# Optimization experiments

Measured on AMD Instinct MI355X. Metric: run time of the kernel, lower is better.

Reference implementation:

```python
import jax, jax.numpy as jnp
import numpy as np

D_MODEL = 1024
N_HEADS = 16
D_HEAD = D_MODEL // N_HEADS
B, T = 4, 2048


def setup_inputs() -> dict:
    key = jax.random.key(0)
    ks = jax.random.split(key, 7)
    s = 0.02
    q = jax.random.normal(ks[0], (B, T, D_MODEL), dtype=jnp.float32)
    k = jax.random.normal(ks[1], (B, T, D_MODEL), dtype=jnp.float32)
    v = jax.random.normal(ks[2], (B, T, D_MODEL), dtype=jnp.float32)
    # causal mask, True = masked (strict upper triangle)
    mask = jnp.triu(jnp.ones((T, T), dtype=bool), k=1)[None, None, :, :]
    Wq = jax.random.normal(ks[3], (D_MODEL, D_MODEL), dtype=jnp.float32) * s
    Wk = jax.random.normal(ks[4], (D_MODEL, D_MODEL), dtype=jnp.float32) * s
    Wv = jax.random.normal(ks[5], (D_MODEL, D_MODEL), dtype=jnp.float32) * s
    Wo = jax.random.normal(ks[6], (D_MODEL, D_MODEL), dtype=jnp.float32) * s
    return {"q": q, "k": k, "v": v, "mask": mask,
            "Wq": Wq, "Wk": Wk, "Wv": Wv, "Wo": Wo}


def reference(q, k, v, mask, Wq, Wk, Wv, Wo):
    H, Dh = N_HEADS, D_HEAD
    scale = Dh ** -0.5

    def split(t):  # [B,T,D] -> [B,H,T,Dh]
        Bt, Tt, _ = t.shape
        return t.reshape(Bt, Tt, H, Dh).transpose(0, 2, 1, 3)

    # torch Linear (no bias): y = x @ W.T
    Q = split(q @ Wq.T)
    K = split(k @ Wk.T)
    V = split(v @ Wv.T)

    scores = jnp.einsum('bhqd,bhkd->bhqk', Q, K) * scale
    scores = jnp.where(mask, -jnp.inf, scores)
    attn = jax.nn.softmax(scores, axis=-1)
    attn = jnp.nan_to_num(attn)  # fully-masked rows -> 0
    out = jnp.einsum('bhqk,bhkd->bhqd', attn, V)
    out = out.transpose(0, 2, 1, 3).reshape(q.shape[0], q.shape[1], H * Dh)
    return out @ Wo.T
```

## Files before the change

kernel.cpp:

```cpp
#include <hip/hip_runtime.h>
#include <stdint.h>

#define D_MODEL 1024
#define N_HEADS 16
#define D_HEAD 64
#define BATCH 4
#define SEQ 2048
#define MTOT (BATCH * SEQ)

typedef unsigned short u16;
typedef __attribute__((ext_vector_type(8))) short bf16x8;
typedef __attribute__((ext_vector_type(4))) float f32x4;

#define MFMA(a, b, c) __builtin_amdgcn_mfma_f32_16x16x32_bf16((a), (b), (c), 0, 0, 0)
#define LOG2E 1.4426950408889634f
#define SC (0.125f * LOG2E)

static __device__ __forceinline__ u16 f2bf(float f) {
  unsigned u = __builtin_bit_cast(unsigned, f);
  u += 0x7fffu + ((u >> 16) & 1u);
  return (u16)(u >> 16);
}
static __device__ __forceinline__ u16 f2bf_t(float f) {
  return (u16)(__builtin_bit_cast(unsigned, f) >> 16);
}

static __device__ __forceinline__ void gload_lds16(const void* g, void* l) {
  __builtin_amdgcn_global_load_lds(
      (const __attribute__((address_space(1))) void*)g,
      (__attribute__((address_space(3))) void*)l, 16, 0, 0);
}

__global__ __launch_bounds__(256) void cvt3(const float* __restrict__ a,
                                            const float* __restrict__ b,
                                            const float* __restrict__ c,
                                            u16* __restrict__ oa, u16* __restrict__ ob,
                                            u16* __restrict__ oc) {
  const int z = blockIdx.y;
  const float* in = (z == 0) ? a : (z == 1) ? b : c;
  u16* out = (z == 0) ? oa : (z == 1) ? ob : oc;
  int i = blockIdx.x * 256 + threadIdx.x;
  float4 v = ((const float4*)in)[i];
  ushort4 o;
  o.x = f2bf(v.x); o.y = f2bf(v.y); o.z = f2bf(v.z); o.w = f2bf(v.w);
  ((ushort4*)out)[i] = o;
}

__global__ __launch_bounds__(256) void cvt4(const float* __restrict__ a,
                                            const float* __restrict__ b,
                                            const float* __restrict__ c,
                                            const float* __restrict__ d,
                                            u16* __restrict__ oa, u16* __restrict__ ob,
                                            u16* __restrict__ oc, u16* __restrict__ od) {
  const int z = blockIdx.y;
  const float* in = (z == 0) ? a : (z == 1) ? b : (z == 2) ? c : d;
  u16* out = (z == 0) ? oa : (z == 1) ? ob : (z == 2) ? oc : od;
  const float s = (z == 0) ? SC : 1.0f;
  int i = blockIdx.x * 256 + threadIdx.x;
  float4 v = ((const float4*)in)[i];
  ushort4 o;
  o.x = f2bf(v.x * s); o.y = f2bf(v.y * s); o.z = f2bf(v.z * s); o.w = f2bf(v.w * s);
  ((ushort4*)out)[i] = o;
}

#define BM 256
#define BN 128
#define BK 64
#define NKT (D_MODEL / BK)
#define ASZ (BM * BK)
#define BSZ (BN * BK)

static __device__ __forceinline__ void gemm_core(const u16* __restrict__ A,
                                                 const u16* __restrict__ B,
                                                 u16* As, u16* Bs,
                                                 int m0, int n0, f32x4 acc[4][4]) {
  const int t = threadIdx.x;
  const int lane = t & 63, wave = t >> 6;
  const int wm = wave >> 1, wn = wave & 1;
  const int lrow = lane & 15, quad = lane >> 4;
  const int srow = t >> 3;
  const int swcol = (((t & 7) ^ (srow & 7)) << 3);
  const int sdst = srow * 64 + (t & 7) * 8;
  const int rsw = lrow & 7;

#pragma unroll
  for (int i = 0; i < 4; i++)
#pragma unroll
    for (int j = 0; j < 4; j++) acc[i][j] = (f32x4){0.f, 0.f, 0.f, 0.f};

#define STAGE_(kt_, bi_)                                                        \
  do {                                                                          \
    const int k0_ = (kt_)*BK;                                                   \
    u16* as_ = As + (bi_)*ASZ;                                                  \
    u16* bs_ = Bs + (bi_)*BSZ;                                                  \
    _Pragma("unroll") for (int r_ = 0; r_ < 4; ++r_)                            \
        gload_lds16(A + (size_t)(m0 + r_ * 64 + srow) * 1024 + k0_ + swcol,     \
                    as_ + r_ * 64 * 64 + sdst);                                 \
    _Pragma("unroll") for (int r_ = 0; r_ < 2; ++r_)                            \
        gload_lds16(B + (size_t)(n0 + r_ * 64 + srow) * 1024 + k0_ + swcol,     \
                    bs_ + r_ * 64 * 64 + sdst);                                 \
  } while (0)

  STAGE_(0, 0);
  STAGE_(1, 1);

  for (int kt = 0; kt < NKT; ++kt) {
    if (kt < NKT - 1) asm volatile("s_waitcnt vmcnt(6)" ::: "memory");
    else              asm volatile("s_waitcnt vmcnt(0)" ::: "memory");
    __builtin_amdgcn_s_barrier();
    asm volatile("" ::: "memory");

    if (kt + 2 < NKT) STAGE_(kt + 2, (kt + 2) % 3);

    const u16* as = As + (kt % 3) * ASZ;
    const u16* bs = Bs + (kt % 3) * BSZ;

    bf16x8 a[2][4], b[2][4];
#pragma unroll
    for (int ks = 0; ks < 2; ++ks) {
      const int cx = ((ks * 4 + quad) ^ rsw) << 3;
#pragma unroll
      for (int i = 0; i < 4; i++)
        a[ks][i] = *(const bf16x8*)(as + (wm * 64 + i * 16 + lrow) * 64 + cx);
#pragma unroll
      for (int j = 0; j < 4; j++)
        b[ks][j] = *(const bf16x8*)(bs + (wn * 64 + j * 16 + lrow) * 64 + cx);
    }
#pragma unroll
    for (int ks = 0; ks < 2; ++ks) {
      __builtin_amdgcn_s_setprio(1);
#pragma unroll
      for (int i = 0; i < 4; i++)
#pragma unroll
        for (int j = 0; j < 4; j++) acc[i][j] = MFMA(a[ks][i], b[ks][j], acc[i][j]);
      __builtin_amdgcn_s_setprio(0);
    }
    __builtin_amdgcn_sched_barrier(0);
  }
#undef STAGE_
}

__global__ __launch_bounds__(512, 2) void gemm_qkv(const u16* __restrict__ xq,
                                                   const u16* __restrict__ xk,
                                                   const u16* __restrict__ xv,
                                                   const u16* __restrict__ Wqb,
                                                   const u16* __restrict__ Wkb,
                                                   const u16* __restrict__ Wvb,
                                                   u16* __restrict__ Qb, u16* __restrict__ Kb,
                                                   u16* __restrict__ Vtg, int zbase) {
  __shared__ u16 As[3 * ASZ];
  __shared__ u16 Bs[3 * BSZ];
  const int z = blockIdx.z + zbase;
  const u16* A = (z == 0) ? xq : (z == 1) ? xk : xv;
  const u16* B = (z == 0) ? Wqb : (z == 1) ? Wkb : Wvb;
  const int m0 = blockIdx.x * BM, n0 = blockIdx.y * BN;

  f32x4 acc[4][4];
  gemm_core(A, B, As, Bs, m0, n0, acc);

  const int lane = threadIdx.x & 63, wave = threadIdx.x >> 6;
  const int wm = wave >> 1, wn = wave & 1;
  const int lrow = lane & 15, quad = lane >> 4;

  if (z == 2) {
    const int b = m0 >> 11;
    const int t0 = (m0 & 2047);
#pragma unroll
    for (int i = 0; i < 4; i++) {
      const int trow = t0 + wm * 64 + i * 16 + quad * 4;
#pragma unroll
      for (int j = 0; j < 4; j++) {
        const int n = n0 + wn * 64 + j * 16 + lrow;
        ushort4 pk;
        pk.x = f2bf(acc[i][j][0]); pk.y = f2bf(acc[i][j][1]);
        pk.z = f2bf(acc[i][j][2]); pk.w = f2bf(acc[i][j][3]);
        *(ushort4*)(Vtg + (size_t)b * D_MODEL * SEQ + (size_t)n * SEQ + trow) = pk;
      }
    }
  } else {
    u16* C = z ? Kb : Qb;
#pragma unroll
    for (int i = 0; i < 4; i++) {
      const int mr = m0 + wm * 64 + i * 16 + quad * 4;
#pragma unroll
      for (int j = 0; j < 4; j++) {
        const int n = n0 + wn * 64 + j * 16 + lrow;
#pragma unroll
        for (int r = 0; r < 4; r++) C[(size_t)(mr + r) * 1024 + n] = f2bf(acc[i][j][r]);
      }
    }
  }
}

__global__ __launch_bounds__(512, 2) void gemm_o(const u16* __restrict__ A,
                                                 const u16* __restrict__ B,
                                                 float* __restrict__ C) {
  __shared__ u16 As[3 * ASZ];
  __shared__ u16 Bs[3 * BSZ];
  const int m0 = blockIdx.x * BM, n0 = blockIdx.y * BN;

  f32x4 acc[4][4];
  gemm_core(A, B, As, Bs, m0, n0, acc);

  const int lane = threadIdx.x & 63, wave = threadIdx.x >> 6;
  const int wm = wave >> 1, wn = wave & 1;
  const int lrow = lane & 15, quad = lane >> 4;
#pragma unroll
  for (int i = 0; i < 4; i++) {
    const int mr = m0 + wm * 64 + i * 16 + quad * 4;
#pragma unroll
    for (int j = 0; j < 4; j++) {
      const int n = n0 + wn * 64 + j * 16 + lrow;
#pragma unroll
      for (int r = 0; r < 4; r++) C[(size_t)(mr + r) * 1024 + n] = acc[i][j][r];
    }
  }
}

__global__ __launch_bounds__(256) void attn_causal(const u16* __restrict__ Qb,
                                                   const u16* __restrict__ Kb,
                                                   const u16* __restrict__ Vtg,
                                                   u16* __restrict__ Ob) {
  __shared__ u16 QPs[128 * 64];
  __shared__ u16 Ks[3 * 64 * 64];
  __shared__ u16 Vs[3 * 64 * 64];

  const int t = threadIdx.x;
  const int lane = t & 63, wave = t >> 6;
  const int lrow = lane & 15, quad = lane >> 4;
  const int wb = wave * 32;
  const int bh = blockIdx.x;
  const int b = bh >> 4, h = bh & 15;
  const int col0 = h * 64;
  const size_t rowbase = (size_t)b * SEQ;
  const size_t vbase = (size_t)b * (size_t)D_MODEL * SEQ;
  const int srow = t >> 3;
  const int swcol = (((t & 7) ^ (srow & 7)) << 3);
  const int pchunk = (t & 7) * 8;
  const int rsw = lrow & 7;

#define KVSTAGE_(kt_, bi_)                                                      \
  do {                                                                          \
    const int j0_ = (kt_)*64;                                                   \
    u16* ks_ = Ks + (bi_)*4096;                                                 \
    u16* vs_ = Vs + (bi_)*4096;                                                 \
    _Pragma("unroll") for (int r_ = 0; r_ < 2; ++r_) {                          \
      int rr_ = r_ * 32 + srow;                                                 \
      gload_lds16(Kb + (rowbase + j0_ + rr_) * D_MODEL + col0 + swcol,          \
                  ks_ + rr_ * 64 + pchunk);                                     \
      gload_lds16(Vtg + vbase + (size_t)(col0 + rr_) * SEQ + j0_ + swcol,       \
                  vs_ + rr_ * 64 + pchunk);                                     \
    }                                                                           \
  } while (0)

  bf16x8 bOnes;
  {
    const short ov = (lrow == 0) ? (short)0x3F80 : (short)0;
#pragma unroll
    for (int e = 0; e < 8; ++e) bOnes[e] = ov;
  }

  for (int part = 0; part < 2; ++part) {
    const int qt = part ? (15 - (int)blockIdx.y) : (int)blockIdx.y;
    const int qrow0 = qt * 128;
    const int nkt = 2 * qt + 2;

#pragma unroll
    for (int r = 0; r < 4; ++r) {
      int rr = r * 32 + srow;
      gload_lds16(Qb + (rowbase + qrow0 + rr) * D_MODEL + col0 + swcol,
                  QPs + rr * 64 + pchunk);
    }
    KVSTAGE_(0, 0);
    KVSTAGE_(1, 1);

    bf16x8 bQ[2][2];
    f32x4 oacc[2][4];
    f32x4 lacc[2];
#pragma unroll
    for (int mf = 0; mf < 2; mf++) {
#pragma unroll
      for (int df = 0; df < 4; df++) oacc[mf][df] = (f32x4){0.f, 0.f, 0.f, 0.f};
      lacc[mf] = (f32x4){0.f, 0.f, 0.f, 0.f};
    }

    for (int kt = 0; kt < nkt; ++kt) {
      if (kt < nkt - 1) asm volatile("s_waitcnt vmcnt(4)" ::: "memory");
      else              asm volatile("s_waitcnt vmcnt(0)" ::: "memory");
      __builtin_amdgcn_s_barrier();
      asm volatile("" ::: "memory");

      if (kt + 2 < nkt) KVSTAGE_(kt + 2, (kt + 2) % 3);

      const u16* ksb = Ks + (kt % 3) * 4096;
      const u16* vsb = Vs + (kt % 3) * 4096;

      if (kt == 0) {
#pragma unroll
        for (int mf = 0; mf < 2; ++mf)
#pragma unroll
          for (int ks = 0; ks < 2; ++ks)
            bQ[mf][ks] = *(const bf16x8*)(QPs + (wb + mf * 16 + lrow) * 64 +
                                          (((ks * 4 + quad) ^ rsw) << 3));
      }

      const int j0 = kt * 64;
      const bool diag = (kt >= 2 * qt);
#pragma unroll
      for (int mf = 0; mf < 2; ++mf) {
        f32x4 st[4];
#pragma unroll
        for (int jf = 0; jf < 4; jf++) st[jf] = (f32x4){0.f, 0.f, 0.f, 0.f};
#pragma unroll
        for (int ks = 0; ks < 2; ++ks) {
          const int cx = ((ks * 4 + quad) ^ rsw) << 3;
#pragma unroll
          for (int jf = 0; jf < 4; jf++) {
            bf16x8 aK = *(const bf16x8*)(ksb + (jf * 16 + lrow) * 64 + cx);
            st[jf] = MFMA(aK, bQ[mf][ks], st[jf]);
          }
        }
        const int m = wb + mf * 16 + lrow;
        const int gm = qrow0 + m;
#pragma unroll
        for (int jf = 0; jf < 4; jf++) {
          ushort4 pk;
#pragma unroll
          for (int r = 0; r < 4; r++) {
            float p = __builtin_amdgcn_exp2f(st[jf][r]);
            const int gj = j0 + jf * 16 + quad * 4 + r;
            if (diag && gj > gm) p = 0.f;
            ((u16*)&pk)[r] = f2bf_t(p);
          }
          const int j = jf * 16 + quad * 4;
          *(ushort4*)(QPs + m * 64 + ((((j >> 3) ^ (m & 7)) << 3) | (j & 7))) = pk;
        }
      }

#pragma unroll
      for (int ks = 0; ks < 2; ++ks) {
        const int cx = ((ks * 4 + quad) ^ rsw) << 3;
        bf16x8 aP[2];
#pragma unroll
        for (int mf = 0; mf < 2; ++mf)
          aP[mf] = *(const bf16x8*)(QPs + (wb + mf * 16 + lrow) * 64 + cx);
        lacc[0] = MFMA(aP[0], bOnes, lacc[0]);
        lacc[1] = MFMA(aP[1], bOnes, lacc[1]);
#pragma unroll
        for (int df = 0; df < 4; df++) {
          bf16x8 bV = *(const bf16x8*)(vsb + (df * 16 + lrow) * 64 + cx);
          oacc[0][df] = MFMA(aP[0], bV, oacc[0][df]);
          oacc[1][df] = MFMA(aP[1], bV, oacc[1][df]);
        }
      }
      __builtin_amdgcn_sched_barrier(0);
    }
    __syncthreads();

    float linv[2][4];
#pragma unroll
    for (int mf = 0; mf < 2; mf++)
#pragma unroll
      for (int r = 0; r < 4; r++)
        linv[mf][r] = 1.0f / __shfl(lacc[mf][r], lane & 48);

#pragma unroll
    for (int mf = 0; mf < 2; mf++)
#pragma unroll
      for (int r = 0; r < 4; r++) {
        u16* orow = Ob + (rowbase + qrow0 + wb + mf * 16 + quad * 4 + r) * D_MODEL + col0;
#pragma unroll
        for (int df = 0; df < 4; df++)
          orow[df * 16 + lrow] = f2bf(oacc[mf][df][r] * linv[mf][r]);
      }
  }
#undef KVSTAGE_
}

extern "C" void kernel_launch(void* const* d_in, const int* in_sizes, int n_in,
                              void* d_out, int out_size, void* d_ws, size_t ws_size,
                              hipStream_t stream) {
  const float* q  = (const float*)d_in[0];
  const float* k  = (const float*)d_in[1];
  const float* v  = (const float*)d_in[2];
  const float* Wq = (const float*)d_in[4];
  const float* Wk = (const float*)d_in[5];
  const float* Wv = (const float*)d_in[6];
  const float* Wo = (const float*)d_in[7];
  float* out = (float*)d_out;

  char* ws = (char*)d_ws;
  const size_t MB = 1 << 20;
  u16* xq  = (u16*)(ws);
  u16* xk  = (u16*)(ws + 16 * MB);
  u16* xv  = (u16*)(ws + 32 * MB);
  u16* Wqb = (u16*)(ws + 48 * MB);
  u16* Wkb = (u16*)(ws + 50 * MB);
  u16* Wvb = (u16*)(ws + 52 * MB);
  u16* Wob = (u16*)(ws + 54 * MB);
  u16* Qb  = (u16*)(ws + 56 * MB);

  const dim3 cb(256);
  const dim3 gb(512);
  cvt3<<<dim3(MTOT * D_MODEL / 4 / 256, 3), cb, 0, stream>>>(q, k, v, xq, xk, xv);
  cvt4<<<dim3(D_MODEL * D_MODEL / 4 / 256, 4), cb, 0, stream>>>(Wq, Wk, Wv, Wo,
                                                                Wqb, Wkb, Wvb, Wob);

  if (ws_size >= 104 * MB) {
    u16* Kb  = (u16*)(ws + 72 * MB);
    u16* Vtg = (u16*)(ws + 88 * MB);
    gemm_qkv<<<dim3(32, 8, 3), gb, 0, stream>>>(xq, xk, xv, Wqb, Wkb, Wvb,
                                                Qb, Kb, Vtg, 0);
    attn_causal<<<dim3(64, 8), cb, 0, stream>>>(Qb, Kb, Vtg, xq);
    gemm_o<<<dim3(32, 8), gb, 0, stream>>>(xq, Wob, out);
  } else {
    u16* Kb  = (u16*)(ws);
    u16* Vtg = (u16*)(ws + 16 * MB);
    u16* Oatt = (u16*)(ws + 32 * MB);
    gemm_qkv<<<dim3(32, 8, 1), gb, 0, stream>>>(xq, xq, xq, Wqb, Wqb, Wqb,
                                                Qb, Qb, Qb, 0);
    gemm_qkv<<<dim3(32, 8, 1), gb, 0, stream>>>(xk, xk, xk, Wkb, Wkb, Wkb,
                                                Kb, Kb, Kb, 1);
    gemm_qkv<<<dim3(32, 8, 1), gb, 0, stream>>>(xv, xv, xv, Wvb, Wvb, Wvb,
                                                Vtg, Vtg, Vtg, 2);
    attn_causal<<<dim3(64, 8), cb, 0, stream>>>(Qb, Kb, Vtg, Oatt);
    gemm_o<<<dim3(32, 8), gb, 0, stream>>>(Oatt, Wob, out);
  }
}
```

Measured before the change: 319.2 us.

## Fuse fp32-to-bf16 activation conversion into QKV GEMM A-tile loading

Removes the separate cvt3 pass over q/k/v. The QKV GEMM now loads fp32 activations straight into registers, converts them with packed bf16 conversion instructions and writes them to LDS, while the weights still arrive via direct-to-LDS loads. This saves a full read and write of 96MB of activation traffic and a kernel launch. To fit the register-staged A path, the pipeline drops from triple to double buffering in both GEMMs, and the bf16 GEMM adds an extra barrier before staging. In exchange it adds register pressure and less latency hiding in the GEMMs, and the workspace-size fallback path is removed.

```diff
diff --git a/kernel.cpp b/kernel.cpp
--- a/kernel.cpp
+++ b/kernel.cpp
@@ -24,26 +24,16 @@
 static __device__ __forceinline__ u16 f2bf_t(float f) {
   return (u16)(__builtin_bit_cast(unsigned, f) >> 16);
 }
+static __device__ __forceinline__ unsigned cvtpk(float lo, float hi) {
+  unsigned r;
+  asm volatile("v_cvt_pk_bf16_f32 %0, %1, %2" : "=v"(r) : "v"(lo), "v"(hi));
+  return r;
+}
 
 static __device__ __forceinline__ void gload_lds16(const void* g, void* l) {
   __builtin_amdgcn_global_load_lds(
       (const __attribute__((address_space(1))) void*)g,
       (__attribute__((address_space(3))) void*)l, 16, 0, 0);
-}
-
-__global__ __launch_bounds__(256) void cvt3(const float* __restrict__ a,
-                                            const float* __restrict__ b,
-                                            const float* __restrict__ c,
-                                            u16* __restrict__ oa, u16* __restrict__ ob,
-                                            u16* __restrict__ oc) {
-  const int z = blockIdx.y;
-  const float* in = (z == 0) ? a : (z == 1) ? b : c;
-  u16* out = (z == 0) ? oa : (z == 1) ? ob : oc;
-  int i = blockIdx.x * 256 + threadIdx.x;
-  float4 v = ((const float4*)in)[i];
-  ushort4 o;
-  o.x = f2bf(v.x); o.y = f2bf(v.y); o.z = f2bf(v.z); o.w = f2bf(v.w);
-  ((ushort4*)out)[i] = o;
 }
 
 __global__ __launch_bounds__(256) void cvt4(const float* __restrict__ a,
@@ -110,53 +100,141 @@
     __builtin_amdgcn_s_barrier();
     asm volatile("" ::: "memory");
 
-    if (kt + 2 < NKT) STAGE_(kt + 2, (kt + 2) % 3);
-
-    const u16* as = As + (kt % 3) * ASZ;
-    const u16* bs = Bs + (kt % 3) * BSZ;
-
-    bf16x8 a[2][4], b[2][4];
+    const u16* as = As + (kt & 1) * ASZ;
+    const u16* bs = Bs + (kt & 1) * BSZ;
+
 #pragma unroll
     for (int ks = 0; ks < 2; ++ks) {
       const int cx = ((ks * 4 + quad) ^ rsw) << 3;
+      bf16x8 a[4], b[4];
 #pragma unroll
       for (int i = 0; i < 4; i++)
-        a[ks][i] = *(const bf16x8*)(as + (wm * 64 + i * 16 + lrow) * 64 + cx);
+        a[i] = *(const bf16x8*)(as + (wm * 64 + i * 16 + lrow) * 64 + cx);
 #pragma unroll
       for (int j = 0; j < 4; j++)
-        b[ks][j] = *(const bf16x8*)(bs + (wn * 64 + j * 16 + lrow) * 64 + cx);
-    }
+        b[j] = *(const bf16x8*)(bs + (wn * 64 + j * 16 + lrow) * 64 + cx);
+      __builtin_amdgcn_s_setprio(1);
+#pragma unroll
+      for (int i = 0; i < 4; i++)
+#pragma unroll
+        for (int j = 0; j < 4; j++) acc[i][j] = MFMA(a[i], b[j], acc[i][j]);
+      __builtin_amdgcn_s_setprio(0);
+    }
+
+    if (kt + 2 < NKT) {
+      asm volatile("" ::: "memory");
+      __builtin_amdgcn_sched_barrier(0);
+      __builtin_amdgcn_s_barrier();
+      STAGE_(kt + 2, kt & 1);
+    }
+  }
+#undef STAGE_
+}
+
+static __device__ __forceinline__ void gemm_core_f32A(const float* __restrict__ A,
+                                                      const u16* __restrict__ B,
+                                                      u16* As, u16* Bs,
+                                                      int m0, int n0, f32x4 acc[4][4]) {
+  const int t = threadIdx.x;
+  const int lane = t & 63, wave = t >> 6;
+  const int wm = wave >> 1, wn = wave & 1;
+  const int lrow = lane & 15, quad = lane >> 4;
+  const int srow = t >> 3;
+  const int swcol = (((t & 7) ^ (srow & 7)) << 3);
+  const int sdst = srow * 64 + (t & 7) * 8;
+  const int rsw = lrow & 7;
+
+#pragma unroll
+  for (int i = 0; i < 4; i++)
+#pragma unroll
+    for (int j = 0; j < 4; j++) acc[i][j] = (f32x4){0.f, 0.f, 0.f, 0.f};
+
+  float4 af[4][2];
+
+#define ALOAD_(kt_)                                                             \
+  do {                                                                          \
+    _Pragma("unroll") for (int r_ = 0; r_ < 4; ++r_) {                          \
+      const float* ap_ = A + (size_t)(m0 + r_ * 64 + srow) * 1024 + (kt_)*BK + swcol; \
+      af[r_][0] = *(const float4*)ap_;                                          \
+      af[r_][1] = *(const float4*)(ap_ + 4);                                    \
+    }                                                                           \
+  } while (0)
+
+#define AWRITE_(bi_)                                                            \
+  do {                                                                          \
+    _Pragma("unroll") for (int r_ = 0; r_ < 4; ++r_) {                          \
+      uint4 w_;                                                                 \
+      w_.x = cvtpk(af[r_][0].x, af[r_][0].y);                                   \
+      w_.y = cvtpk(af[r_][0].z, af[r_][0].w);                                   \
+      w_.z = cvtpk(af[r_][1].x, af[r_][1].y);                                   \
+      w_.w = cvtpk(af[r_][1].z, af[r_][1].w);                                   \
+      *(uint4*)(As + (bi_)*ASZ + r_ * 4096 + sdst) = w_;                        \
+    }                                                                           \
+  } while (0)
+
+#define BSTAGE_(kt_, bi_)                                                       \
+  do {                                                                          \
+    _Pragma("unroll") for (int r_ = 0; r_ < 2; ++r_)                            \
+        gload_lds16(B + (size_t)(n0 + r_ * 64 + srow) * 1024 + (kt_)*BK + swcol,\
+                    Bs + (bi_)*BSZ + r_ * 4096 + sdst);                         \
+  } while (0)
+
+  ALOAD_(0);
+  BSTAGE_(0, 0);
+  AWRITE_(0);
+  __syncthreads();
+
+  for (int kt = 0; kt < NKT; ++kt) {
+    const bool pf = (kt + 1 < NKT);
+    if (pf) { ALOAD_(kt + 1); BSTAGE_(kt + 1, (kt + 1) & 1); }
+    __builtin_amdgcn_sched_barrier(0);
+
+    const u16* as = As + (kt & 1) * ASZ;
+    const u16* bs = Bs + (kt & 1) * BSZ;
+
 #pragma unroll
     for (int ks = 0; ks < 2; ++ks) {
+      const int cx = ((ks * 4 + quad) ^ rsw) << 3;
+      bf16x8 a[4], b[4];
+#pragma unroll
+      for (int i = 0; i < 4; i++)
+        a[i] = *(const bf16x8*)(as + (wm * 64 + i * 16 + lrow) * 64 + cx);
+#pragma unroll
+      for (int j = 0; j < 4; j++)
+        b[j] = *(const bf16x8*)(bs + (wn * 64 + j * 16 + lrow) * 64 + cx);
       __builtin_amdgcn_s_setprio(1);
 #pragma unroll
       for (int i = 0; i < 4; i++)
 #pragma unroll
-        for (int j = 0; j < 4; j++) acc[i][j] = MFMA(a[ks][i], b[ks][j], acc[i][j]);
+        for (int j = 0; j < 4; j++) acc[i][j] = MFMA(a[i], b[j], acc[i][j]);
       __builtin_amdgcn_s_setprio(0);
     }
-    __builtin_amdgcn_sched_barrier(0);
-  }
-#undef STAGE_
-}
-
-__global__ __launch_bounds__(512, 2) void gemm_qkv(const u16* __restrict__ xq,
-                                                   const u16* __restrict__ xk,
-                                                   const u16* __restrict__ xv,
+
+    if (pf) AWRITE_((kt + 1) & 1);
+    __syncthreads();
+  }
+#undef ALOAD_
+#undef AWRITE_
+#undef BSTAGE_
+}
+
+__global__ __launch_bounds__(512, 2) void gemm_qkv(const float* __restrict__ q,
+                                                   const float* __restrict__ k,
+                                                   const float* __restrict__ v,
                                                    const u16* __restrict__ Wqb,
                                                    const u16* __restrict__ Wkb,
                                                    const u16* __restrict__ Wvb,
                                                    u16* __restrict__ Qb, u16* __restrict__ Kb,
-                                                   u16* __restrict__ Vtg, int zbase) {
-  __shared__ u16 As[3 * ASZ];
-  __shared__ u16 Bs[3 * BSZ];
-  const int z = blockIdx.z + zbase;
-  const u16* A = (z == 0) ? xq : (z == 1) ? xk : xv;
+                                                   u16* __restrict__ Vtg) {
+  __shared__ u16 As[2 * ASZ];
+  __shared__ u16 Bs[2 * BSZ];
+  const int z = blockIdx.z;
+  const float* A = (z == 0) ? q : (z == 1) ? k : v;
   const u16* B = (z == 0) ? Wqb : (z == 1) ? Wkb : Wvb;
   const int m0 = blockIdx.x * BM, n0 = blockIdx.y * BN;
 
   f32x4 acc[4][4];
-  gemm_core(A, B, As, Bs, m0, n0, acc);
+  gemm_core_f32A(A, B, As, Bs, m0, n0, acc);
 
   const int lane = threadIdx.x & 63, wave = threadIdx.x >> 6;
   const int wm = wave >> 1, wn = wave & 1;
@@ -195,8 +273,8 @@
 __global__ __launch_bounds__(512, 2) void gemm_o(const u16* __restrict__ A,
                                                  const u16* __restrict__ B,
                                                  float* __restrict__ C) {
-  __shared__ u16 As[3 * ASZ];
-  __shared__ u16 Bs[3 * BSZ];
+  __shared__ u16 As[2 * ASZ];
+  __shared__ u16 Bs[2 * BSZ];
   const int m0 = blockIdx.x * BM, n0 = blockIdx.y * BN;
 
   f32x4 acc[4][4];
@@ -391,39 +469,20 @@
 
   char* ws = (char*)d_ws;
   const size_t MB = 1 << 20;
-  u16* xq  = (u16*)(ws);
-  u16* xk  = (u16*)(ws + 16 * MB);
-  u16* xv  = (u16*)(ws + 32 * MB);
-  u16* Wqb = (u16*)(ws + 48 * MB);
-  u16* Wkb = (u16*)(ws + 50 * MB);
-  u16* Wvb = (u16*)(ws + 52 * MB);
-  u16* Wob = (u16*)(ws + 54 * MB);
-  u16* Qb  = (u16*)(ws + 56 * MB);
+  u16* Kb   = (u16*)(ws);
+  u16* Vtg  = (u16*)(ws + 16 * MB);
+  u16* Oatt = (u16*)(ws + 32 * MB);
+  u16* Wqb  = (u16*)(ws + 48 * MB);
+  u16* Wkb  = (u16*)(ws + 50 * MB);
+  u16* Wvb  = (u16*)(ws + 52 * MB);
+  u16* Wob  = (u16*)(ws + 54 * MB);
+  u16* Qb   = (u16*)(ws + 56 * MB);
 
   const dim3 cb(256);
   const dim3 gb(512);
-  cvt3<<<dim3(MTOT * D_MODEL / 4 / 256, 3), cb, 0, stream>>>(q, k, v, xq, xk, xv);
   cvt4<<<dim3(D_MODEL * D_MODEL / 4 / 256, 4), cb, 0, stream>>>(Wq, Wk, Wv, Wo,
                                                                 Wqb, Wkb, Wvb, Wob);
-
-  if (ws_size >= 104 * MB) {
-    u16* Kb  = (u16*)(ws + 72 * MB);
-    u16* Vtg = (u16*)(ws + 88 * MB);
-    gemm_qkv<<<dim3(32, 8, 3), gb, 0, stream>>>(xq, xk, xv, Wqb, Wkb, Wvb,
-                                                Qb, Kb, Vtg, 0);
-    attn_causal<<<dim3(64, 8), cb, 0, stream>>>(Qb, Kb, Vtg, xq);
-    gemm_o<<<dim3(32, 8), gb, 0, stream>>>(xq, Wob, out);
-  } else {
-    u16* Kb  = (u16*)(ws);
-    u16* Vtg = (u16*)(ws + 16 * MB);
-    u16* Oatt = (u16*)(ws + 32 * MB);
-    gemm_qkv<<<dim3(32, 8, 1), gb, 0, stream>>>(xq, xq, xq, Wqb, Wqb, Wqb,
-                                                Qb, Qb, Qb, 0);
-    gemm_qkv<<<dim3(32, 8, 1), gb, 0, stream>>>(xk, xk, xk, Wkb, Wkb, Wkb,
-                                                Kb, Kb, Kb, 1);
-    gemm_qkv<<<dim3(32, 8, 1), gb, 0, stream>>>(xv, xv, xv, Wvb, Wvb, Wvb,
-                                                Vtg, Vtg, Vtg, 2);
-    attn_causal<<<dim3(64, 8), cb, 0, stream>>>(Qb, Kb, Vtg, Oatt);
-    gemm_o<<<dim3(32, 8), gb, 0, stream>>>(Oatt, Wob, out);
-  }
-}
+  gemm_qkv<<<dim3(32, 8, 3), gb, 0, stream>>>(q, k, v, Wqb, Wkb, Wvb, Qb, Kb, Vtg);
+  attn_causal<<<dim3(64, 8), cb, 0, stream>>>(Qb, Kb, Vtg, Oatt);
+  gemm_o<<<dim3(32, 8), gb, 0, stream>>>(Oatt, Wob, out);
+}
```

New measurement: 341.0 us. 6.8% more time.
